# Optimization experiments

Hardware: AMD Instinct MI355X
Metric: run time of the kernel (lower is better)

Reference implementation:

```python
import jax, jax.numpy as jnp
import numpy as np

SAMPLE_RATE = 24000
THRESHOLD_FACTOR = 5.0
MAX_SPIKE_SAMPLES = int(0.0015 * SAMPLE_RATE)  # 36
K_MAX = 65536  # static upper bound on number of threshold crossings
N_SAMPLES = 24_000_000


def setup_inputs() -> dict:
    key = jax.random.key(0)
    x = jax.random.normal(key, (N_SAMPLES,), dtype=jnp.float32)
    return {"data_detected": x}


def _detect_one(v, threshold):
    """Detect peaks of v above +threshold. For the negative pass, call with -x
    (x < -thr  <=>  -x > thr, and argmin(x) == argmax(-x)). Returns an int32
    array of length K_MAX: valid peak indices first (sorted), padded with -1."""
    N = v.shape[0]
    mask = (v > threshold).astype(jnp.int32)
    d = jnp.diff(mask)  # +1 = entry (False->True), -1 = exit (True->False)
    entries = jnp.nonzero(d == 1, size=K_MAX, fill_value=N)[0]
    exits = jnp.nonzero(d == -1, size=K_MAX, fill_value=N)[0]
    n = jnp.minimum(jnp.sum(d == 1), jnp.sum(d == -1))
    idx = jnp.arange(K_MAX)
    dur = exits - entries
    keep = (idx < n) & (dur <= MAX_SPIKE_SAMPLES)
    # vectorized windowed peak search: (K_MAX, W) gather + row argmax
    win_idx = jnp.clip(entries[:, None] + jnp.arange(MAX_SPIKE_SAMPLES)[None, :], 0, N - 1)
    windows = v[win_idx]
    peaks = entries + jnp.argmax(windows, axis=1)
    # compact valid peaks to the front (entries are sorted), pad with -1
    peaks = jnp.sort(jnp.where(keep, peaks, N))
    total = jnp.sum(keep)
    return jnp.where(idx < total, peaks, -1)


def reference(data_detected):
    x = data_detected
    threshold = THRESHOLD_FACTOR * jnp.median(jnp.abs(x)) / 0.6745
    pos_indices = _detect_one(x, threshold)
    neg_indices = _detect_one(-x, threshold)
    return pos_indices, neg_indices, threshold
```

## Files before the change

### kernel.cpp

```cpp
#include <hip/hip_runtime.h>
#include <stdint.h>

#define HB 18
#define SH_SIZE 8192
#define NSAMP 65536
#define SMARG 1912
#define DBITS 22
#define CAND_CAP 8192
#define CSORT_CAP 4096
#define CBUF_CAP 256
#define LIST_CAP 2500000
#define LBUF_CAP 4096
#define PAIR_CAP 512
#define PEAK_CAP 512
#define MAX_SPIKE 36
#define AB_BLOCKS 128
#define MAIN_BLOCKS 1024

#define P_ULO   0
#define P_UHI   1
#define P_THRLO 2
#define P_THR   3
#define P_CANDN 4
#define P_LISTN 5
#define P_CB    6
#define P_BINA1 7
#define P_BINA2 8
#define P_RA1   9
#define P_RA2   10
#define P_DONES 11
#define P_DONEA 12
#define P_DONEB 13

#define WS_SHIST  0
#define WS_HISTA  32768
#define WS_HISTB  40960
#define WS_PARAMS 57344
#define WS_ZERO_BYTES 57408
#define WS_CAND   57600
#define WS_LIST   102400

__global__ __launch_bounds__(256) void k_prep(int* __restrict__ ws, int nInts,
                                              float* __restrict__ out, int n2) {
  int j = blockIdx.x * 256 + threadIdx.x;
  if (j < nInts) ws[j] = 0;
  if (j < n2) out[j] = -1.0f;
}

__global__ __launch_bounds__(256) void k_sample(const float* __restrict__ x, int N,
                                                int* __restrict__ shist,
                                                int* __restrict__ p) {
  __shared__ int h[SH_SIZE];
  __shared__ int lastS;
  __shared__ int part[256];
  __shared__ int excl[256];
  __shared__ uint32_t uLoS, uHiS;
  int tid = threadIdx.x;
  for (int i = tid; i < SH_SIZE; i += 256) h[i] = 0;
  __syncthreads();
  int stride = N / NSAMP; if (stride < 1) stride = 1;
  for (int i = blockIdx.x * 256 + tid; i < NSAMP; i += gridDim.x * 256) {
    long long idx = (long long)i * stride;
    if (idx < N) {
      uint32_t u = __float_as_uint(x[idx]) & 0x7fffffffu;
      atomicAdd(&h[u >> HB], 1);
    }
  }
  __syncthreads();
  for (int i = tid; i < SH_SIZE; i += 256) {
    int c = h[i];
    if (c) atomicAdd(&shist[i], c);
  }
  __threadfence();
  if (tid == 0) lastS = (atomicAdd(&p[P_DONES], 1) == (int)gridDim.x - 1);
  __syncthreads();
  if (!lastS) return;
  __threadfence();
  const int chunk = SH_SIZE / 256;
  int base = tid * chunk;
  int s = 0;
  int cc[chunk];
  for (int w = 0; w < chunk; ++w) { cc[w] = shist[base + w]; s += cc[w]; }
  part[tid] = s;
  __syncthreads();
  if (tid == 0) { int a = 0; for (int i = 0; i < 256; ++i) { excl[i] = a; a += part[i]; } }
  __syncthreads();
  int pre = excl[tid];
  int sA = NSAMP / 2 - SMARG, sB = NSAMP / 2 + SMARG;
  if (pre <= sA && sA < pre + s) {
    int a = pre;
    for (int w = 0; w < chunk; ++w) {
      if (sA < a + cc[w]) { uLoS = (uint32_t)(base + w) << HB; break; }
      a += cc[w];
    }
  }
  if (pre <= sB && sB < pre + s) {
    int a = pre;
    for (int w = 0; w < chunk; ++w) {
      if (sB < a + cc[w]) { uHiS = (uint32_t)(base + w + 1) << HB; break; }
      a += cc[w];
    }
  }
  __syncthreads();
  if (tid == 0) {
    uint32_t uLo = uLoS, uHi = uHiS;
    if (uHi - uLo > (1u << DBITS)) uHi = uLo + (1u << DBITS);
    p[P_ULO] = (int)uLo;
    p[P_UHI] = (int)uHi;
    float vLo = __uint_as_float(uLo);
    p[P_THRLO] = __float_as_int((5.0f * vLo / 0.6745f) * 0.999f);
  }
}

__device__ __forceinline__ void m_elem(uint32_t fbits, int idx, uint32_t uLo, uint32_t bw,
                                       uint32_t thrBits, int* lbuf, int* lcnt,
                                       int* cbuf, int* ccnt, int& cb) {
  uint32_t u = fbits & 0x7fffffffu;
  cb += (u < uLo) ? 1 : 0;
  if (u - uLo < bw) {
    int id = atomicAdd(lcnt, 1);
    if (id < LBUF_CAP) lbuf[id] = (int)(u - uLo);
  }
  if (u > thrBits) {
    int id = atomicAdd(ccnt, 1);
    if (id < CBUF_CAP) cbuf[id] = idx;
  }
}

__global__ __launch_bounds__(256) void k_main(const float* __restrict__ x, int N,
                                              int* __restrict__ p,
                                              int* __restrict__ list,
                                              int* __restrict__ cand) {
  __shared__ int lbuf[LBUF_CAP];
  __shared__ int cbuf[CBUF_CAP];
  __shared__ int red[256];
  __shared__ int lcnt, ccnt, lbase, cbase;
  int tid = threadIdx.x;
  if (tid == 0) { lcnt = 0; ccnt = 0; }
  __syncthreads();
  uint32_t uLo = (uint32_t)p[P_ULO];
  uint32_t bw  = (uint32_t)p[P_UHI] - uLo;
  uint32_t thrBits = (uint32_t)p[P_THRLO];
  int cb = 0;
  int NV = N >> 2;
  int nTiles = NV >> 11;
  const uint4* vec = reinterpret_cast<const uint4*>(x);
  for (int t = blockIdx.x; t < nTiles; t += gridDim.x) {
    const uint4* bp = vec + ((long long)t << 11) + tid;
    uint4 v0 = bp[0];
    uint4 v1 = bp[256];
    uint4 v2 = bp[512];
    uint4 v3 = bp[768];
    uint4 v4 = bp[1024];
    uint4 v5 = bp[1280];
    uint4 v6 = bp[1536];
    uint4 v7 = bp[1792];
    asm volatile("" ::: "memory");
    int eb = (t << 13) + (tid << 2);
#define PROC(vk, koff)                                                              \
    m_elem(vk.x, eb + (koff) + 0, uLo, bw, thrBits, lbuf, &lcnt, cbuf, &ccnt, cb);  \
    m_elem(vk.y, eb + (koff) + 1, uLo, bw, thrBits, lbuf, &lcnt, cbuf, &ccnt, cb);  \
    m_elem(vk.z, eb + (koff) + 2, uLo, bw, thrBits, lbuf, &lcnt, cbuf, &ccnt, cb);  \
    m_elem(vk.w, eb + (koff) + 3, uLo, bw, thrBits, lbuf, &lcnt, cbuf, &ccnt, cb)
    PROC(v0, 0);
    PROC(v1, 1024);
    PROC(v2, 2048);
    PROC(v3, 3072);
    PROC(v4, 4096);
    PROC(v5, 5120);
    PROC(v6, 6144);
    PROC(v7, 7168);
#undef PROC
  }
  for (int j = (nTiles << 11) + blockIdx.x * 256 + tid; j < NV; j += gridDim.x * 256) {
    uint4 a = vec[j];
    int ei = j << 2;
    m_elem(a.x, ei + 0, uLo, bw, thrBits, lbuf, &lcnt, cbuf, &ccnt, cb);
    m_elem(a.y, ei + 1, uLo, bw, thrBits, lbuf, &lcnt, cbuf, &ccnt, cb);
    m_elem(a.z, ei + 2, uLo, bw, thrBits, lbuf, &lcnt, cbuf, &ccnt, cb);
    m_elem(a.w, ei + 3, uLo, bw, thrBits, lbuf, &lcnt, cbuf, &ccnt, cb);
  }
  if (blockIdx.x == 0 && tid == 0) {
    for (int i2 = NV << 2; i2 < N; ++i2)
      m_elem(__float_as_uint(x[i2]), i2, uLo, bw, thrBits, lbuf, &lcnt, cbuf, &ccnt, cb);
  }
  __syncthreads();
  int nl = lcnt < LBUF_CAP ? lcnt : LBUF_CAP;
  int nc = ccnt < CBUF_CAP ? ccnt : CBUF_CAP;
  if (tid == 0) {
    lbase = atomicAdd(&p[P_LISTN], nl);
    cbase = atomicAdd(&p[P_CANDN], nc);
  }
  red[tid] = cb;
  __syncthreads();
  for (int s2 = 128; s2; s2 >>= 1) {
    if (tid < s2) red[tid] += red[tid + s2];
    __syncthreads();
  }
  if (tid == 0) atomicAdd(&p[P_CB], red[0]);
  for (int i2 = tid; i2 < nl; i2 += 256)
    if (lbase + i2 < LIST_CAP) list[lbase + i2] = lbuf[i2];
  for (int i2 = tid; i2 < nc; i2 += 256)
    if (cbase + i2 < CAND_CAP) cand[cbase + i2] = cbuf[i2];
}

__global__ __launch_bounds__(256) void k_stageA(const int* __restrict__ list,
                                                int* __restrict__ p,
                                                int* __restrict__ histA, int N) {
  __shared__ int h[2048];
  __shared__ int lastS;
  __shared__ int part[256];
  __shared__ int excl[256];
  int tid = threadIdx.x;
  for (int i = tid; i < 2048; i += 256) h[i] = 0;
  __syncthreads();
  int n = p[P_LISTN]; if (n > LIST_CAP) n = LIST_CAP;
  int str = gridDim.x * 256;
  for (int i = blockIdx.x * 256 + tid; i < n; i += str)
    atomicAdd(&h[list[i] >> 11], 1);
  __syncthreads();
  for (int i = tid; i < 2048; i += 256) {
    int c = h[i];
    if (c) atomicAdd(&histA[i], c);
  }
  __threadfence();
  if (tid == 0) lastS = (atomicAdd(&p[P_DONEA], 1) == (int)gridDim.x - 1);
  __syncthreads();
  if (!lastS) return;
  __threadfence();
  long long k1 = (long long)(N / 2) - 1, k2 = (long long)(N / 2);
  long long cb = p[P_CB];
  long long r1l = k1 - cb, r2l = k2 - cb;
  if (r1l < 0) r1l = 0; if (r1l > n - 1) r1l = n - 1;
  if (r2l < 0) r2l = 0; if (r2l > n - 1) r2l = n - 1;
  int r1 = (int)r1l, r2 = (int)r2l;
  int base = tid * 8;
  int cc[8]; int s = 0;
#pragma unroll
  for (int w = 0; w < 8; ++w) { cc[w] = histA[base + w]; s += cc[w]; }
  part[tid] = s;
  __syncthreads();
  if (tid == 0) { int a = 0; for (int i = 0; i < 256; ++i) { excl[i] = a; a += part[i]; } }
  __syncthreads();
  int pre = excl[tid];
  if (pre <= r1 && r1 < pre + s) {
    int a = pre;
    for (int w = 0; w < 8; ++w) {
      if (r1 < a + cc[w]) { p[P_BINA1] = base + w; p[P_RA1] = r1 - a; break; }
      a += cc[w];
    }
  }
  if (pre <= r2 && r2 < pre + s) {
    int a = pre;
    for (int w = 0; w < 8; ++w) {
      if (r2 < a + cc[w]) { p[P_BINA2] = base + w; p[P_RA2] = r2 - a; break; }
      a += cc[w];
    }
  }
}

__device__ static void isort(int* a, int n) {
  for (int i = 1; i < n; ++i) {
    int v = a[i]; int j = i - 1;
    while (j >= 0 && a[j] > v) { a[j + 1] = a[j]; --j; }
    a[j + 1] = v;
  }
}

__device__ inline void eval_pair(const float* __restrict__ x, int p, float thr,
                                 int* pe, int* px, int* ne, int* nx, int* cnt) {
  float a = x[p], b = x[p + 1];
  bool m0 = a > thr, m1 = b > thr;
  if (m0 != m1) {
    int id = atomicAdd(&cnt[m1 ? 0 : 1], 1);
    if (id < PAIR_CAP) (m1 ? pe : px)[id] = p;
  }
  bool q0 = (-a) > thr, q1 = (-b) > thr;
  if (q0 != q1) {
    int id = atomicAdd(&cnt[q1 ? 2 : 3], 1);
    if (id < PAIR_CAP) (q1 ? ne : nx)[id] = p;
  }
}

__device__ inline int wave_argmax36(const float* __restrict__ x, int N, int sign,
                                    int e, int lane) {
  float val = -INFINITY;
  int wi = lane;
  if (lane < MAX_SPIKE) {
    int idx = e + lane; if (idx > N - 1) idx = N - 1;
    float v = x[idx];
    val = (sign < 0) ? -v : v;
  }
  for (int off = 32; off; off >>= 1) {
    float ov = __shfl_xor(val, off);
    int owi = __shfl_xor(wi, off);
    if (ov > val || (ov == val && owi < wi)) { val = ov; wi = owi; }
  }
  return e + wi;
}

__device__ inline int proc_pol(const float* __restrict__ x, int N, int sign,
                               const int* eL, int nE, const int* xL, int nX,
                               int* pk, int lane) {
  int n = nE < nX ? nE : nX;
  int tot = 0;
  for (int t = 0; t < n; ++t) {
    int dur = xL[t] - eL[t];
    if (dur <= MAX_SPIKE) {
      int pp = wave_argmax36(x, N, sign, eL[t], lane);
      if (tot < PEAK_CAP && lane == 0) pk[tot] = pp;
      ++tot;
    }
  }
  if (tot > PEAK_CAP) tot = PEAK_CAP;
  if (lane == 0) isort(pk, tot);
  return tot;
}

__global__ __launch_bounds__(256) void k_stageB(const float* __restrict__ x, int N,
                                                const int* __restrict__ list,
                                                int* __restrict__ p,
                                                int* __restrict__ histB,
                                                int* __restrict__ cand,
                                                float* __restrict__ out, int OUT_K) {
  __shared__ int h[4096];
  __shared__ int lastS;
  __shared__ int part[256];
  __shared__ int excl[256];
  __shared__ float vres[2];
  __shared__ float sthr;
  __shared__ int cl[CSORT_CAP];
  __shared__ int pe[PAIR_CAP], px[PAIR_CAP], ne[PAIR_CAP], nx[PAIR_CAP];
  __shared__ int cnt[4];
  __shared__ int pkP[PEAK_CAP], pkN[PEAK_CAP];
  __shared__ int nPk[2];
  int tid = threadIdx.x;
  for (int i = tid; i < 4096; i += 256) h[i] = 0;
  __syncthreads();
  int n = p[P_LISTN]; if (n > LIST_CAP) n = LIST_CAP;
  int binA1 = p[P_BINA1], binA2 = p[P_BINA2];
  int str = gridDim.x * 256;
  for (int i = blockIdx.x * 256 + tid; i < n; i += str) {
    int d = list[i];
    int hi = d >> 11, lo = d & 2047;
    if (hi == binA1) atomicAdd(&h[lo], 1);
    if (hi == binA2) atomicAdd(&h[2048 + lo], 1);
  }
  __syncthreads();
  for (int i = tid; i < 4096; i += 256) {
    int c = h[i];
    if (c) atomicAdd(&histB[i], c);
  }
  __threadfence();
  if (tid == 0) lastS = (atomicAdd(&p[P_DONEB], 1) == (int)gridDim.x - 1);
  __syncthreads();
  if (!lastS) return;
  __threadfence();
  uint32_t uLo = (uint32_t)p[P_ULO];
  if (tid < 2) vres[tid] = __uint_as_float(uLo);
  for (int tgt = 0; tgt < 2; ++tgt) {
    __syncthreads();
    const int* hh = histB + tgt * 2048;
    int rank = (tgt == 0) ? p[P_RA1] : p[P_RA2];
    int binA = (tgt == 0) ? binA1 : binA2;
    int base = tid * 8;
    int cc[8]; int s = 0;
#pragma unroll
    for (int w = 0; w < 8; ++w) { cc[w] = hh[base + w]; s += cc[w]; }
    part[tid] = s;
    __syncthreads();
    if (tid == 0) { int a = 0; for (int i = 0; i < 256; ++i) { excl[i] = a; a += part[i]; } }
    __syncthreads();
    int pre = excl[tid];
    if (pre <= rank && rank < pre + s) {
      int a = pre;
      for (int w = 0; w < 8; ++w) {
        if (rank < a + cc[w]) {
          uint32_t bits = uLo + ((uint32_t)binA << 11) + (uint32_t)(base + w);
          vres[tgt] = __uint_as_float(bits);
          break;
        }
        a += cc[w];
      }
    }
  }
  __syncthreads();
  if (tid == 0) {
    float med = 0.5f * (vres[0] + vres[1]);
    float thr = (5.0f * med) / 0.6745f;
    p[P_THR] = __float_as_int(thr);
    sthr = thr;
    out[2 * OUT_K] = thr;
  }
  if (tid < 4) cnt[tid] = 0;
  __syncthreads();
  float thr = sthr;
  int nC = p[P_CANDN]; if (nC > CAND_CAP) nC = CAND_CAP;
  const int* cnd;
  if (nC <= CSORT_CAP) {
    for (int i = tid; i < nC; i += 256) cl[i] = cand[i];
    __syncthreads();
    int myv[CSORT_CAP / 256], myr[CSORT_CAP / 256], nh = 0;
    for (int i = tid; i < nC; i += 256) {
      int v = cl[i];
      int r = 0;
      for (int q = 0; q < nC; ++q) r += (cl[q] < v) ? 1 : 0;
      myv[nh] = v; myr[nh] = r; ++nh;
    }
    __syncthreads();
    for (int t = 0; t < nh; ++t) cl[myr[t]] = myv[t];
    __syncthreads();
    cnd = cl;
  } else {
    if (tid == 0) isort(cand, nC);
    __syncthreads();
    cnd = cand;
  }
  for (int k = tid; k < nC; k += 256) {
    int c = cnd[k];
    bool prevAdj = (k > 0) && (cnd[k - 1] == c - 1);
    if (c > 0 && !prevAdj) eval_pair(x, c - 1, thr, pe, px, ne, nx, cnt);
    if (c <= N - 2) eval_pair(x, c, thr, pe, px, ne, nx, cnt);
  }
  __syncthreads();
  int nPE = min(cnt[0], PAIR_CAP), nPX = min(cnt[1], PAIR_CAP);
  int nNE = min(cnt[2], PAIR_CAP), nNX = min(cnt[3], PAIR_CAP);
  if (tid == 0) { isort(pe, nPE); isort(px, nPX); }
  else if (tid == 1) { isort(ne, nNE); isort(nx, nNX); }
  __syncthreads();
  if (tid < 64) {
    int t0 = proc_pol(x, N, +1, pe, nPE, px, nPX, pkP, tid);
    int t1 = proc_pol(x, N, -1, ne, nNE, nx, nNX, pkN, tid);
    if (tid == 0) { nPk[0] = t0; nPk[1] = t1; }
  }
  __syncthreads();
  for (int j = tid; j < nPk[0]; j += 256) out[j] = (float)pkP[j];
  for (int j = tid; j < nPk[1]; j += 256) out[OUT_K + j] = (float)pkN[j];
}

extern "C" void kernel_launch(void* const* d_in, const int* in_sizes, int n_in,
                              void* d_out, int out_size, void* d_ws, size_t ws_size,
                              hipStream_t stream) {
  const float* x = (const float*)d_in[0];
  int N = in_sizes[0];
  float* out = (float*)d_out;
  char* ws = (char*)d_ws;

  int* shist  = (int*)(ws + WS_SHIST);
  int* histA  = (int*)(ws + WS_HISTA);
  int* histB  = (int*)(ws + WS_HISTB);
  int* params = (int*)(ws + WS_PARAMS);
  int* cand   = (int*)(ws + WS_CAND);
  int* list   = (int*)(ws + WS_LIST);

  int OUT_K = (out_size - 1) / 2;
  int nInts = WS_ZERO_BYTES / 4;
  int prepN = 2 * OUT_K;

  k_prep<<<(prepN + 255) / 256, 256, 0, stream>>>((int*)ws, nInts, out, prepN);
  k_sample<<<64, 256, 0, stream>>>(x, N, shist, params);
  k_main<<<MAIN_BLOCKS, 256, 0, stream>>>(x, N, params, list, cand);
  k_stageA<<<AB_BLOCKS, 256, 0, stream>>>(list, params, histA, N);
  k_stageB<<<AB_BLOCKS, 256, 0, stream>>>(x, N, list, params, histB, cand, out, OUT_K);
}
```

Baseline: 141.1 us.

## Fuse stage-A median histogram into main pass and retune grid and sampling

Moves the stage-A coarse histogram of in-band values into k_main, built from each block's shared-memory buffer. The last-finishing block then finds the median bins, so the separate k_stageA launch and its re-read of the global list go away. The grid sizes for the main and stage-B kernels are doubled, the local list buffer and sampling margin are shrunk, and the sampler now reads the first 65536 contiguous samples instead of strided ones. The contiguous sampling and tighter margin depend on the input being stationary noise, which makes the selection band less robust on other data.

```diff
diff --git a/kernel.cpp b/kernel.cpp
--- a/kernel.cpp
+++ b/kernel.cpp
@@ -4,18 +4,18 @@
 #define HB 18
 #define SH_SIZE 8192
 #define NSAMP 65536
-#define SMARG 1912
+#define SMARG 800
 #define DBITS 22
 #define CAND_CAP 8192
 #define CSORT_CAP 4096
 #define CBUF_CAP 256
 #define LIST_CAP 2500000
-#define LBUF_CAP 4096
+#define LBUF_CAP 3072
 #define PAIR_CAP 512
 #define PEAK_CAP 512
 #define MAX_SPIKE 36
-#define AB_BLOCKS 128
-#define MAIN_BLOCKS 1024
+#define B_BLOCKS 256
+#define MAIN_G 2048
 
 #define P_ULO   0
 #define P_UHI   1
@@ -58,11 +58,9 @@
   int tid = threadIdx.x;
   for (int i = tid; i < SH_SIZE; i += 256) h[i] = 0;
   __syncthreads();
-  int stride = N / NSAMP; if (stride < 1) stride = 1;
   for (int i = blockIdx.x * 256 + tid; i < NSAMP; i += gridDim.x * 256) {
-    long long idx = (long long)i * stride;
-    if (idx < N) {
-      uint32_t u = __float_as_uint(x[idx]) & 0x7fffffffu;
+    if (i < N) {
+      uint32_t u = __float_as_uint(x[i]) & 0x7fffffffu;
       atomicAdd(&h[u >> HB], 1);
     }
   }
@@ -130,13 +128,17 @@
 __global__ __launch_bounds__(256) void k_main(const float* __restrict__ x, int N,
                                               int* __restrict__ p,
                                               int* __restrict__ list,
-                                              int* __restrict__ cand) {
+                                              int* __restrict__ cand,
+                                              int* __restrict__ histA) {
   __shared__ int lbuf[LBUF_CAP];
   __shared__ int cbuf[CBUF_CAP];
+  __shared__ int histA_l[2048];
   __shared__ int red[256];
-  __shared__ int lcnt, ccnt, lbase, cbase;
+  __shared__ int excl[256];
+  __shared__ int lcnt, ccnt, lbase, cbase, lastS;
   int tid = threadIdx.x;
   if (tid == 0) { lcnt = 0; ccnt = 0; }
+  for (int i = tid; i < 2048; i += 256) histA_l[i] = 0;
   __syncthreads();
   uint32_t uLo = (uint32_t)p[P_ULO];
   uint32_t bw  = (uint32_t)p[P_UHI] - uLo;
@@ -155,7 +157,6 @@
     uint4 v5 = bp[1280];
     uint4 v6 = bp[1536];
     uint4 v7 = bp[1792];
-    asm volatile("" ::: "memory");
     int eb = (t << 13) + (tid << 2);
 #define PROC(vk, koff)                                                              \
     m_elem(vk.x, eb + (koff) + 0, uLo, bw, thrBits, lbuf, &lcnt, cbuf, &ccnt, cb);  \
@@ -187,50 +188,37 @@
   __syncthreads();
   int nl = lcnt < LBUF_CAP ? lcnt : LBUF_CAP;
   int nc = ccnt < CBUF_CAP ? ccnt : CBUF_CAP;
+  for (int i = tid; i < nl; i += 256)
+    atomicAdd(&histA_l[(lbuf[i] >> 11) & 2047], 1);
+  red[tid] = cb;
+  __syncthreads();
+  for (int s2 = 128; s2; s2 >>= 1) {
+    if (tid < s2) red[tid] += red[tid + s2];
+    __syncthreads();
+  }
   if (tid == 0) {
     lbase = atomicAdd(&p[P_LISTN], nl);
     cbase = atomicAdd(&p[P_CANDN], nc);
-  }
-  red[tid] = cb;
-  __syncthreads();
-  for (int s2 = 128; s2; s2 >>= 1) {
-    if (tid < s2) red[tid] += red[tid + s2];
-    __syncthreads();
-  }
-  if (tid == 0) atomicAdd(&p[P_CB], red[0]);
-  for (int i2 = tid; i2 < nl; i2 += 256)
-    if (lbase + i2 < LIST_CAP) list[lbase + i2] = lbuf[i2];
-  for (int i2 = tid; i2 < nc; i2 += 256)
-    if (cbase + i2 < CAND_CAP) cand[cbase + i2] = cbuf[i2];
-}
-
-__global__ __launch_bounds__(256) void k_stageA(const int* __restrict__ list,
-                                                int* __restrict__ p,
-                                                int* __restrict__ histA, int N) {
-  __shared__ int h[2048];
-  __shared__ int lastS;
-  __shared__ int part[256];
-  __shared__ int excl[256];
-  int tid = threadIdx.x;
-  for (int i = tid; i < 2048; i += 256) h[i] = 0;
-  __syncthreads();
+    atomicAdd(&p[P_CB], red[0]);
+  }
+  __syncthreads();
+  for (int i = tid; i < nl; i += 256)
+    if (lbase + i < LIST_CAP) list[lbase + i] = lbuf[i];
+  for (int i = tid; i < nc; i += 256)
+    if (cbase + i < CAND_CAP) cand[cbase + i] = cbuf[i];
+  for (int i = tid; i < 2048; i += 256) {
+    int c = histA_l[i];
+    if (c) atomicAdd(&histA[i], c);
+  }
+  __threadfence();
+  if (tid == 0) lastS = (atomicAdd(&p[P_DONEA], 1) == (int)gridDim.x - 1);
+  __syncthreads();
+  if (!lastS) return;
+  __threadfence();
   int n = p[P_LISTN]; if (n > LIST_CAP) n = LIST_CAP;
-  int str = gridDim.x * 256;
-  for (int i = blockIdx.x * 256 + tid; i < n; i += str)
-    atomicAdd(&h[list[i] >> 11], 1);
-  __syncthreads();
-  for (int i = tid; i < 2048; i += 256) {
-    int c = h[i];
-    if (c) atomicAdd(&histA[i], c);
-  }
-  __threadfence();
-  if (tid == 0) lastS = (atomicAdd(&p[P_DONEA], 1) == (int)gridDim.x - 1);
-  __syncthreads();
-  if (!lastS) return;
-  __threadfence();
   long long k1 = (long long)(N / 2) - 1, k2 = (long long)(N / 2);
-  long long cb = p[P_CB];
-  long long r1l = k1 - cb, r2l = k2 - cb;
+  long long cbAll = p[P_CB];
+  long long r1l = k1 - cbAll, r2l = k2 - cbAll;
   if (r1l < 0) r1l = 0; if (r1l > n - 1) r1l = n - 1;
   if (r2l < 0) r2l = 0; if (r2l > n - 1) r2l = n - 1;
   int r1 = (int)r1l, r2 = (int)r2l;
@@ -238,9 +226,9 @@
   int cc[8]; int s = 0;
 #pragma unroll
   for (int w = 0; w < 8; ++w) { cc[w] = histA[base + w]; s += cc[w]; }
-  part[tid] = s;
-  __syncthreads();
-  if (tid == 0) { int a = 0; for (int i = 0; i < 256; ++i) { excl[i] = a; a += part[i]; } }
+  red[tid] = s;
+  __syncthreads();
+  if (tid == 0) { int a = 0; for (int i = 0; i < 256; ++i) { excl[i] = a; a += red[i]; } }
   __syncthreads();
   int pre = excl[tid];
   if (pre <= r1 && r1 < pre + s) {
@@ -459,7 +447,6 @@
 
   k_prep<<<(prepN + 255) / 256, 256, 0, stream>>>((int*)ws, nInts, out, prepN);
   k_sample<<<64, 256, 0, stream>>>(x, N, shist, params);
-  k_main<<<MAIN_BLOCKS, 256, 0, stream>>>(x, N, params, list, cand);
-  k_stageA<<<AB_BLOCKS, 256, 0, stream>>>(list, params, histA, N);
-  k_stageB<<<AB_BLOCKS, 256, 0, stream>>>(x, N, list, params, histB, cand, out, OUT_K);
-}
+  k_main<<<MAIN_G, 256, 0, stream>>>(x, N, params, list, cand, histA);
+  k_stageB<<<B_BLOCKS, 256, 0, stream>>>(x, N, list, params, histB, cand, out, OUT_K);
+}
```

New measurement: 263.1 us. +86.5%, slower.
